# Performance work log

Measured on AMD Instinct MI355X. Metric: run time of the kernel, lower is better.

## Reference

```python
import jax, jax.numpy as jnp
import numpy as np

B, L, D = 32, 1024, 768          # batch, max wordpiece len, hidden size
C, K = 256, 8                    # max_chunk_number, max_chunk_len
PAD = 1                          # conv1d padding (kernel 3)


def setup_inputs() -> dict:
    key = jax.random.key(0)
    k1, k2, k3, k4 = jax.random.split(key, 4)
    token_level_features = jax.random.normal(k1, (B, L, D), jnp.float32)
    # values in [0,5): max total length per batch = 256*4 = 1024 = L (always in-bounds)
    chunk_lens = jax.random.randint(k2, (B, C), 0, 5)
    conv_w = jax.random.normal(k3, (D, D, 3), jnp.float32) * 0.02  # (out, in, kernel)
    conv_b = jax.random.normal(k4, (D,), jnp.float32) * 0.02
    return {"token_level_features": token_level_features, "chunk_lens": chunk_lens,
            "conv_w": conv_w, "conv_b": conv_b}


def reference(token_level_features, chunk_lens, conv_w, conv_b):
    Bb, Ll, Dd = token_level_features.shape
    Cc = chunk_lens.shape[1]
    # exclusive cumsum: start wordpiece offset of each chunk (advances by FULL len,
    # even when the chunk is truncated to K, matching the torch loop)
    starts = jnp.cumsum(chunk_lens, axis=1) - chunk_lens          # [B, C]
    trunc = jnp.minimum(chunk_lens, K)                            # [B, C]
    k = jnp.arange(K)
    idx = starts[:, :, None] + k[None, None, :]                   # [B, C, K]
    mask = k[None, None, :] < trunc[:, :, None]                   # [B, C, K]

    # ragged gather -> padded chunk buffer [B, C, K, D]
    bidx = jnp.arange(Bb)[:, None, None]
    gathered = jnp.where(mask[..., None],
                         token_level_features[bidx, jnp.clip(idx, 0, Ll - 1)],
                         0.0)

    # conv1d(k=3, pad=1) + relu over the chunk-length axis (dropout = identity in eval)
    x = gathered.reshape(Bb * Cc, K, Dd).transpose(0, 2, 1)       # [N, D, K]
    y = jax.lax.conv_general_dilated(x, conv_w, (1,), [(PAD, PAD)],
                                     dimension_numbers=('NCH', 'OIH', 'NCH'))
    y = jax.nn.relu(y + conv_b[None, :, None])
    y = y.transpose(0, 2, 1).reshape(Bb, Cc, K, Dd)               # [B, C, K, D]

    # scatter back to wordpiece positions; masked slots go to dump row L (discarded)
    safe_scatter = jnp.where(mask, idx, Ll)
    out = jnp.zeros((Bb, Ll + 1, Dd), token_level_features.dtype)
    out = out.at[bidx, safe_scatter].set(jnp.where(mask[..., None], y, 0.0))
    return out[:, :Ll]
```

## Files before the change

kernel.cpp:

```cpp
#include <hip/hip_runtime.h>
#include <stdint.h>

constexpr int NB   = 32;
constexpr int LLEN = 1024;
constexpr int DDIM = 768;
constexpr int CCH  = 256;
constexpr int KMAX = 8;
constexpr int KTOT = 3 * DDIM;

constexpr int BM = 128;
constexpr int BN = 128;
constexpr int BK = 64;
constexpr int NKS = KTOT / BK;
constexpr int NTILE = DDIM / BN;
constexpr int NRB = NB * LLEN / BM;

constexpr int CVT_SLICES = 32;
constexpr int ROWS_PER_SLICE = LLEN / CVT_SLICES;

constexpr size_t FLAGS_OFF = 0;
constexpr size_t FLAGS_SZ  = (size_t)NB * LLEN * sizeof(int);
constexpr size_t WP_OFF    = FLAGS_OFF + FLAGS_SZ;
constexpr size_t WP_SZ     = (size_t)NTILE * NKS * BN * BK * 2;
constexpr size_t ZP_OFF    = WP_OFF + WP_SZ;
constexpr size_t ZP_SZ     = 256;
constexpr size_t FB_OFF    = ZP_OFF + ZP_SZ;
constexpr size_t FB_SZ     = (size_t)NB * LLEN * DDIM * 2;
constexpr size_t WS_NEED   = FB_OFF + FB_SZ;

typedef __attribute__((ext_vector_type(4))) float f32x4;
typedef __bf16 bf16x8 __attribute__((ext_vector_type(8)));

__device__ inline unsigned short f2bf(float f) {
    unsigned u = __float_as_uint(f);
    u = u + 0x7FFFu + ((u >> 16) & 1u);
    return (unsigned short)(u >> 16);
}

__device__ inline void gload_lds16(const void* g, void* l) {
    __builtin_amdgcn_global_load_lds(
        (const __attribute__((address_space(1))) unsigned int*)g,
        (__attribute__((address_space(3))) unsigned int*)l, 16, 0, 0);
}

__global__ void meta_kernel(const int* __restrict__ chunk_lens, int* __restrict__ flags) {
    int b = blockIdx.x, tid = threadIdx.x;
    __shared__ int s[CCH];
    int len = chunk_lens[b * CCH + tid];
    s[tid] = len;
    __syncthreads();
    for (int off = 1; off < CCH; off <<= 1) {
        int v = (tid >= off) ? s[tid - off] : 0;
        __syncthreads();
        s[tid] += v;
        __syncthreads();
    }
    int start = s[tid] - len;
    for (int i = tid; i < LLEN; i += CCH) flags[b * LLEN + i] = 0;
    __syncthreads();
    int t = min(len, KMAX);
    for (int k = 0; k < t; ++k) {
        int p = start + k;
        if (p < LLEN)
            flags[b * LLEN + p] = 1 | (k > 0 ? 2 : 0) | (k + 1 < t ? 4 : 0);
    }
}

__global__ void meta_cvt_kernel(const int* __restrict__ chunk_lens,
                                const float* __restrict__ feat,
                                int* __restrict__ flags,
                                unsigned short* __restrict__ featbf) {
    int blk = blockIdx.x;
    int b   = blk / CVT_SLICES;
    int sl  = blk % CVT_SLICES;
    int tid = threadIdx.x;

    __shared__ int s[CCH];
    __shared__ int fl[LLEN];

    int len = chunk_lens[b * CCH + tid];
    s[tid] = len;
    for (int i = tid; i < LLEN; i += 256) fl[i] = 0;
    __syncthreads();
    for (int off = 1; off < CCH; off <<= 1) {
        int v = (tid >= off) ? s[tid - off] : 0;
        __syncthreads();
        s[tid] += v;
        __syncthreads();
    }
    int start = s[tid] - len;
    int t = min(len, KMAX);
    for (int k = 0; k < t; ++k) {
        int p = start + k;
        if (p < LLEN)
            fl[p] = 1 | (k > 0 ? 2 : 0) | (k + 1 < t ? 4 : 0);
    }
    __syncthreads();

    if (sl == 0) {
        for (int i = tid; i < LLEN; i += 256)
            flags[b * LLEN + i] = fl[i];
    }

    constexpr int CH = DDIM / 8;
    int r0 = sl * ROWS_PER_SLICE;
    for (int i = tid; i < ROWS_PER_SLICE * CH; i += 256) {
        int row = r0 + i / CH;
        if (!(fl[row] & 1)) continue;
        int c = i % CH;
        size_t base = ((size_t)(b * LLEN + row)) * DDIM + c * 8;
        f32x4 a  = *reinterpret_cast<const f32x4*>(feat + base);
        f32x4 cc = *reinterpret_cast<const f32x4*>(feat + base + 4);
        uint4 pack;
        pack.x = (unsigned)f2bf(a.x)  | ((unsigned)f2bf(a.y)  << 16);
        pack.y = (unsigned)f2bf(a.z)  | ((unsigned)f2bf(a.w)  << 16);
        pack.z = (unsigned)f2bf(cc.x) | ((unsigned)f2bf(cc.y) << 16);
        pack.w = (unsigned)f2bf(cc.z) | ((unsigned)f2bf(cc.w) << 16);
        *reinterpret_cast<uint4*>(featbf + base) = pack;
    }
}

__global__ void packw2_kernel(const float* __restrict__ conv_w, unsigned short* __restrict__ Wp,
                              unsigned int* __restrict__ zeropage) {
    if (blockIdx.x == gridDim.x - 1) {
        if (threadIdx.x < (int)(ZP_SZ / 4)) zeropage[threadIdx.x] = 0u;
        return;
    }
    int idx = blockIdx.x * 256 + threadIdx.x;
    if (idx >= NTILE * NKS * BN * 8) return;
    int m    = idx & 7;
    int nl   = (idx >> 3) & (BN - 1);
    int rest = idx >> 10;
    int ks   = rest % NKS;
    int nt   = rest / NKS;
    int n    = nt * BN + nl;
    int k0   = ks * BK + m * 8;
    int tap  = k0 / DDIM;
    int i0   = k0 % DDIM;
    const float* src = conv_w + ((size_t)n * DDIM + i0) * 3 + tap;
    unsigned wrds[4];
    #pragma unroll
    for (int j = 0; j < 4; ++j) {
        unsigned lo = f2bf(src[(2 * j) * 3]);
        unsigned hi = f2bf(src[(2 * j + 1) * 3]);
        wrds[j] = lo | (hi << 16);
    }
    size_t dst = ((size_t)(nt * NKS + ks)) * (BN * BK) + nl * BK + 8 * (m ^ (nl & 7));
    *reinterpret_cast<uint4*>(Wp + dst) = make_uint4(wrds[0], wrds[1], wrds[2], wrds[3]);
}

__global__ __launch_bounds__(256, 4) void conv_mfma3_kernel(
    const unsigned short* __restrict__ featbf, const int* __restrict__ flags,
    const unsigned short* __restrict__ Wp, const float* __restrict__ bias,
    const unsigned short* __restrict__ zeropage, float* __restrict__ out)
{
    int s    = blockIdx.x;
    int xcd  = s & 7;
    int slot = s >> 3;
    int b    = slot / NTILE;
    int nt   = slot % NTILE;
    int pblk = (xcd - b) & 7;
    int p0   = pblk * BM;
    int tid  = threadIdx.x;

    __shared__ int s_rf[BM];
    __shared__ int s_any;
    __shared__ float s_bias[BN];
    __shared__ __align__(16) unsigned char As[BM * BK * 2];
    __shared__ __align__(16) unsigned char Bs[BK * BN * 2];

    if (tid == 0) s_any = 0;
    __syncthreads();
    if (tid < BM) {
        int rf = flags[b * LLEN + p0 + tid];
        s_rf[tid] = rf;
        if (rf) atomicOr(&s_any, 1);
    }
    if (tid < BN) s_bias[tid] = bias[nt * BN + tid];
    __syncthreads();

    float* outbase = out + ((size_t)(b * LLEN + p0)) * DDIM + nt * BN;

    if (!s_any) {
        f32x4 z = {0.f, 0.f, 0.f, 0.f};
        #pragma unroll
        for (int q = 0; q < 16; ++q) {
            int flat = q * 256 + tid;
            int row = flat >> 5, c4 = flat & 31;
            *reinterpret_cast<f32x4*>(outbase + (size_t)row * DDIM + c4 * 4) = z;
        }
        return;
    }

    int w  = tid >> 6;
    int l  = tid & 63;
    int wr = w >> 1, wc = w & 1;
    int lr = l & 15, lg = l >> 4;

    int  useq[4];
    const unsigned short* rowptr[4];
    unsigned ldsoff[4];
    #pragma unroll
    for (int q = 0; q < 4; ++q) {
        int flat = q * 256 + tid;
        int row = flat >> 3, c8 = flat & 7;
        int c8s = c8 ^ (row & 7);
        int rf = s_rf[row];
        useq[q] = ((rf >> 1) & 1) | ((rf & 1) << 1) | (((rf >> 2) & 1) << 2);
        rowptr[q] = featbf + ((size_t)(b * LLEN + p0 + row) * DDIM + c8s * 8);
        ldsoff[q] = (unsigned)(((q * 256) + (tid & 192)) * 16);
    }
    const unsigned short* WpBase = Wp + (size_t)nt * NKS * (BN * BK) + (size_t)tid * 8;

    auto stage = [&](int ks) {
        int tap = ks / (DDIM / BK);
        int i0  = (ks % (DDIM / BK)) * BK;
        #pragma unroll
        for (int q = 0; q < 4; ++q) {
            const unsigned short* src = ((useq[q] >> tap) & 1)
                ? rowptr[q] + (size_t)(tap - 1) * DDIM + i0
                : zeropage;
            gload_lds16(src, &As[ldsoff[q]]);
        }
        const unsigned short* bsrc = WpBase + (size_t)ks * (BN * BK);
        #pragma unroll
        for (int q = 0; q < 4; ++q)
            gload_lds16(bsrc + q * 256 * 8, &Bs[ldsoff[q]]);
    };

    f32x4 acc[4][4];
    #pragma unroll
    for (int i = 0; i < 4; ++i)
        #pragma unroll
        for (int j = 0; j < 4; ++j) acc[i][j] = (f32x4){0.f, 0.f, 0.f, 0.f};

    unsigned abase[4], aswz[4], bbase[4], bswz[4];
    #pragma unroll
    for (int fm = 0; fm < 4; ++fm) {
        int row = wr * 64 + fm * 16 + lr;
        abase[fm] = (unsigned)(row * (BK * 2) + lg * 16);
        aswz[fm]  = ((unsigned)(row & 7) << 4);
    }
    #pragma unroll
    for (int fn = 0; fn < 4; ++fn) {
        int col = wc * 64 + fn * 16 + lr;
        bbase[fn] = (unsigned)(col * (BK * 2) + lg * 16);
        bswz[fn]  = ((unsigned)(col & 7) << 4);
    }

    auto compute = [&]() {
        #pragma unroll
        for (int kc = 0; kc < 2; ++kc) {
            bf16x8 av[4], bv[4];
            #pragma unroll
            for (int fm = 0; fm < 4; ++fm)
                av[fm] = *reinterpret_cast<const bf16x8*>(As + ((abase[fm] + kc * 64) ^ aswz[fm]));
            #pragma unroll
            for (int fn = 0; fn < 4; ++fn)
                bv[fn] = *reinterpret_cast<const bf16x8*>(Bs + ((bbase[fn] + kc * 64) ^ bswz[fn]));
            #pragma unroll
            for (int fm = 0; fm < 4; ++fm)
                #pragma unroll
                for (int fn = 0; fn < 4; ++fn)
                    acc[fm][fn] = __builtin_amdgcn_mfma_f32_16x16x32_bf16(
                        av[fm], bv[fn], acc[fm][fn], 0, 0, 0);
        }
    };

    #pragma unroll 1
    for (int ks = 0; ks < NKS; ++ks) {
        stage(ks);
        __syncthreads();
        compute();
        __syncthreads();
    }

    #pragma unroll
    for (int fm = 0; fm < 4; ++fm) {
        #pragma unroll
        for (int fn = 0; fn < 4; ++fn) {
            int colL = wc * 64 + fn * 16 + lr;
            float bn = s_bias[colL];
            #pragma unroll
            for (int j = 0; j < 4; ++j) {
                int rowL = wr * 64 + fm * 16 + lg * 4 + j;
                int rf = s_rf[rowL];
                float v = (rf & 1) ? fmaxf(acc[fm][fn][j] + bn, 0.f) : 0.f;
                outbase[(size_t)rowL * DDIM + colL] = v;
            }
        }
    }
}

__global__ __launch_bounds__(256) void conv_mfma_kernel(
    const float* __restrict__ feat, const int* __restrict__ flags,
    const unsigned short* __restrict__ Wp, const float* __restrict__ bias,
    float* __restrict__ out)
{
    int nt = blockIdx.x % NTILE;
    int rb = blockIdx.x / NTILE;
    int b  = rb / (LLEN / BM);
    int p0 = (rb % (LLEN / BM)) * BM;
    int tid = threadIdx.x;

    __shared__ int s_rf[BM];
    __shared__ int s_any;
    __shared__ float s_bias[BN];
    __shared__ __align__(16) unsigned char As[BM * BK * 2];
    __shared__ __align__(16) unsigned char Bs[BK * BN * 2];

    if (tid == 0) s_any = 0;
    __syncthreads();
    if (tid < BM) {
        int rf = flags[b * LLEN + p0 + tid];
        s_rf[tid] = rf;
        if (rf) atomicOr(&s_any, 1);
    }
    if (tid < BN) s_bias[tid] = bias[nt * BN + tid];
    __syncthreads();

    float* outbase = out + ((size_t)(b * LLEN + p0)) * DDIM + nt * BN;

    if (!s_any) {
        f32x4 z = {0.f, 0.f, 0.f, 0.f};
        #pragma unroll
        for (int q = 0; q < 16; ++q) {
            int flat = q * 256 + tid;
            int row = flat >> 5, c4 = flat & 31;
            *reinterpret_cast<f32x4*>(outbase + (size_t)row * DDIM + c4 * 4) = z;
        }
        return;
    }

    int w  = tid >> 6;
    int l  = tid & 63;
    int wr = w >> 1, wc = w & 1;
    int lr = l & 15, lg = l >> 4;

    f32x4 acc[4][4];
    #pragma unroll
    for (int i = 0; i < 4; ++i)
        #pragma unroll
        for (int j = 0; j < 4; ++j) acc[i][j] = (f32x4){0.f, 0.f, 0.f, 0.f};

    unsigned abase[4], aswz[4], bbase[4], bswz[4];
    #pragma unroll
    for (int fm = 0; fm < 4; ++fm) {
        int row = wr * 64 + fm * 16 + lr;
        abase[fm] = (unsigned)(row * (BK * 2) + lg * 16);
        aswz[fm]  = ((unsigned)(row & 7) << 4);
    }
    #pragma unroll
    for (int fn = 0; fn < 4; ++fn) {
        int col = wc * 64 + fn * 16 + lr;
        bbase[fn] = (unsigned)(col * (BK * 2) + lg * 16);
        bswz[fn]  = ((unsigned)(col & 7) << 4);
    }

    const unsigned short* WpBase = Wp + (size_t)nt * NKS * (BN * BK);

    for (int ks = 0; ks < NKS; ++ks) {
        int tap = ks / (DDIM / BK);
        int i0  = (ks % (DDIM / BK)) * BK;

        #pragma unroll
        for (int q = 0; q < 8; ++q) {
            int flat = q * 256 + tid;
            int row = flat >> 4, c4 = flat & 15;
            int rf = s_rf[row];
            int use = (tap == 0) ? ((rf >> 1) & 1) : (tap == 1) ? (rf & 1) : ((rf >> 2) & 1);
            unsigned lo = 0, hi = 0;
            if (use) {
                int p = p0 + row + tap - 1;
                const float* src = feat + ((size_t)(b * LLEN + p)) * DDIM + i0 + c4 * 4;
                f32x4 v = *reinterpret_cast<const f32x4*>(src);
                lo = (unsigned)f2bf(v.x) | ((unsigned)f2bf(v.y) << 16);
                hi = (unsigned)f2bf(v.z) | ((unsigned)f2bf(v.w) << 16);
            }
            unsigned byte = (unsigned)(row * (BK * 2) + c4 * 8);
            byte ^= ((unsigned)(row & 7) << 4);
            *reinterpret_cast<uint2*>(As + byte) = make_uint2(lo, hi);
        }

        {
            const uint4* src = reinterpret_cast<const uint4*>(WpBase + (size_t)ks * (BN * BK));
            uint4* dst = reinterpret_cast<uint4*>(Bs);
            #pragma unroll
            for (int q = 0; q < 4; ++q) {
                int f16 = q * 256 + tid;
                dst[f16] = src[f16];
            }
        }
        __syncthreads();

        #pragma unroll
        for (int kc = 0; kc < 2; ++kc) {
            bf16x8 av[4], bv[4];
            #pragma unroll
            for (int fm = 0; fm < 4; ++fm)
                av[fm] = *reinterpret_cast<const bf16x8*>(As + ((abase[fm] + kc * 64) ^ aswz[fm]));
            #pragma unroll
            for (int fn = 0; fn < 4; ++fn)
                bv[fn] = *reinterpret_cast<const bf16x8*>(Bs + ((bbase[fn] + kc * 64) ^ bswz[fn]));
            #pragma unroll
            for (int fm = 0; fm < 4; ++fm)
                #pragma unroll
                for (int fn = 0; fn < 4; ++fn)
                    acc[fm][fn] = __builtin_amdgcn_mfma_f32_16x16x32_bf16(
                        av[fm], bv[fn], acc[fm][fn], 0, 0, 0);
        }
        __syncthreads();
    }

    #pragma unroll
    for (int fm = 0; fm < 4; ++fm) {
        #pragma unroll
        for (int fn = 0; fn < 4; ++fn) {
            int colL = wc * 64 + fn * 16 + lr;
            float bn = s_bias[colL];
            #pragma unroll
            for (int j = 0; j < 4; ++j) {
                int rowL = wr * 64 + fm * 16 + lg * 4 + j;
                int rf = s_rf[rowL];
                float v = (rf & 1) ? fmaxf(acc[fm][fn][j] + bn, 0.f) : 0.f;
                outbase[(size_t)rowL * DDIM + colL] = v;
            }
        }
    }
}

extern "C" void kernel_launch(void* const* d_in, const int* in_sizes, int n_in,
                              void* d_out, int out_size, void* d_ws, size_t ws_size,
                              hipStream_t stream) {
    const float* feat = (const float*)d_in[0];
    const int*   lens = (const int*)d_in[1];
    const float* cw   = (const float*)d_in[2];
    const float* cb   = (const float*)d_in[3];
    float* outp = (float*)d_out;

    char* ws = (char*)d_ws;
    int* flags = (int*)(ws + FLAGS_OFF);
    unsigned short* Wp = (unsigned short*)(ws + WP_OFF);
    unsigned int* zeropage = (unsigned int*)(ws + ZP_OFF);

    packw2_kernel<<<(NTILE * NKS * BN * 8 + 255) / 256 + 1, 256, 0, stream>>>(cw, Wp, zeropage);

    if (ws_size >= WS_NEED) {
        unsigned short* featbf = (unsigned short*)(ws + FB_OFF);
        meta_cvt_kernel<<<NB * CVT_SLICES, 256, 0, stream>>>(lens, feat, flags, featbf);
        conv_mfma3_kernel<<<NRB * NTILE, 256, 0, stream>>>(featbf, flags, Wp, cb,
                                                           (const unsigned short*)zeropage, outp);
    } else {
        meta_kernel<<<NB, CCH, 0, stream>>>(lens, flags);
        conv_mfma_kernel<<<NRB * NTILE, 256, 0, stream>>>(feat, flags, Wp, cb, outp);
    }
}
```

Measured before the change: 97.22 us.

## Use 256x256 tiles with double-buffered LDS and interleaved prefetch in conv GEMM

Replaces the 128x128 single-buffered conv GEMM kernel with a 512-thread, 256x256-tile kernel. LDS is double-buffered and next-stage loads are issued in quarter-steps between MFMA groups, gated by vmcnt waits and barriers, with raised wave priority during the MFMA blocks. Weights are repacked for the wider N tile, and the block-to-XCD mapping is reworked. The larger tile cuts operand reloads and exposed load latency, but it lowers occupancy, raises register pressure, and yields a smaller grid (384 blocks), which may leave some compute units idle.

```diff
diff --git a/kernel.cpp b/kernel.cpp
--- a/kernel.cpp
+++ b/kernel.cpp
@@ -15,13 +15,19 @@
 constexpr int NTILE = DDIM / BN;
 constexpr int NRB = NB * LLEN / BM;
 
+constexpr int BM2 = 256;
+constexpr int BN2 = 256;
+constexpr int NKT = KTOT / BK;
+constexpr int NT2 = DDIM / BN2;
+constexpr int NRB2 = NB * (LLEN / BM2) * NT2;
+
 constexpr int CVT_SLICES = 32;
 constexpr int ROWS_PER_SLICE = LLEN / CVT_SLICES;
 
 constexpr size_t FLAGS_OFF = 0;
 constexpr size_t FLAGS_SZ  = (size_t)NB * LLEN * sizeof(int);
 constexpr size_t WP_OFF    = FLAGS_OFF + FLAGS_SZ;
-constexpr size_t WP_SZ     = (size_t)NTILE * NKS * BN * BK * 2;
+constexpr size_t WP_SZ     = (size_t)NT2 * NKT * BN2 * BK * 2;
 constexpr size_t ZP_OFF    = WP_OFF + WP_SZ;
 constexpr size_t ZP_SZ     = 256;
 constexpr size_t FB_OFF    = ZP_OFF + ZP_SZ;
@@ -120,12 +126,7 @@
     }
 }
 
-__global__ void packw2_kernel(const float* __restrict__ conv_w, unsigned short* __restrict__ Wp,
-                              unsigned int* __restrict__ zeropage) {
-    if (blockIdx.x == gridDim.x - 1) {
-        if (threadIdx.x < (int)(ZP_SZ / 4)) zeropage[threadIdx.x] = 0u;
-        return;
-    }
+__global__ void packw2_kernel(const float* __restrict__ conv_w, unsigned short* __restrict__ Wp) {
     int idx = blockIdx.x * 256 + threadIdx.x;
     if (idx >= NTILE * NKS * BN * 8) return;
     int m    = idx & 7;
@@ -149,44 +150,74 @@
     *reinterpret_cast<uint4*>(Wp + dst) = make_uint4(wrds[0], wrds[1], wrds[2], wrds[3]);
 }
 
-__global__ __launch_bounds__(256, 4) void conv_mfma3_kernel(
+__global__ void packw3_kernel(const float* __restrict__ conv_w, unsigned short* __restrict__ Wp2,
+                              unsigned int* __restrict__ zeropage) {
+    if (blockIdx.x == gridDim.x - 1) {
+        if (threadIdx.x < (int)(ZP_SZ / 4)) zeropage[threadIdx.x] = 0u;
+        return;
+    }
+    int idx = blockIdx.x * 256 + threadIdx.x;
+    if (idx >= NT2 * NKT * BN2 * 8) return;
+    int m    = idx & 7;
+    int nl   = (idx >> 3) & (BN2 - 1);
+    int rest = idx >> 11;
+    int ks   = rest % NKT;
+    int nt   = rest / NKT;
+    int n    = nt * BN2 + nl;
+    int k0   = ks * BK + m * 8;
+    int tap  = k0 / DDIM;
+    int i0   = k0 % DDIM;
+    const float* src = conv_w + ((size_t)n * DDIM + i0) * 3 + tap;
+    unsigned wrds[4];
+    #pragma unroll
+    for (int j = 0; j < 4; ++j) {
+        unsigned lo = f2bf(src[(2 * j) * 3]);
+        unsigned hi = f2bf(src[(2 * j + 1) * 3]);
+        wrds[j] = lo | (hi << 16);
+    }
+    size_t dst = ((size_t)(nt * NKT + ks)) * (BN2 * BK) + nl * BK + 8 * (m ^ (nl & 7));
+    *reinterpret_cast<uint4*>(Wp2 + dst) = make_uint4(wrds[0], wrds[1], wrds[2], wrds[3]);
+}
+
+__global__ __launch_bounds__(512, 2) void conv_mfma8_kernel(
     const unsigned short* __restrict__ featbf, const int* __restrict__ flags,
-    const unsigned short* __restrict__ Wp, const float* __restrict__ bias,
+    const unsigned short* __restrict__ Wp2, const float* __restrict__ bias,
     const unsigned short* __restrict__ zeropage, float* __restrict__ out)
 {
     int s    = blockIdx.x;
     int xcd  = s & 7;
     int slot = s >> 3;
-    int b    = slot / NTILE;
-    int nt   = slot % NTILE;
-    int pblk = (xcd - b) & 7;
-    int p0   = pblk * BM;
+    int nt   = slot % NT2;
+    int g    = slot / NT2;
+    int b    = g * 2 + (xcd >> 2);
+    int pblk = ((xcd & 3) + b) & 3;
+    int p0   = pblk * BM2;
     int tid  = threadIdx.x;
 
-    __shared__ int s_rf[BM];
+    __shared__ int s_rf[BM2];
     __shared__ int s_any;
-    __shared__ float s_bias[BN];
-    __shared__ __align__(16) unsigned char As[BM * BK * 2];
-    __shared__ __align__(16) unsigned char Bs[BK * BN * 2];
+    __shared__ float s_bias[BN2];
+    __shared__ __align__(16) unsigned char As[2][BM2 * BK * 2];
+    __shared__ __align__(16) unsigned char Bs[2][BN2 * BK * 2];
 
     if (tid == 0) s_any = 0;
     __syncthreads();
-    if (tid < BM) {
+    if (tid < BM2) {
         int rf = flags[b * LLEN + p0 + tid];
         s_rf[tid] = rf;
         if (rf) atomicOr(&s_any, 1);
     }
-    if (tid < BN) s_bias[tid] = bias[nt * BN + tid];
-    __syncthreads();
-
-    float* outbase = out + ((size_t)(b * LLEN + p0)) * DDIM + nt * BN;
+    if (tid < BN2) s_bias[tid] = bias[nt * BN2 + tid];
+    __syncthreads();
+
+    float* outbase = out + ((size_t)(b * LLEN + p0)) * DDIM + nt * BN2;
 
     if (!s_any) {
         f32x4 z = {0.f, 0.f, 0.f, 0.f};
         #pragma unroll
-        for (int q = 0; q < 16; ++q) {
-            int flat = q * 256 + tid;
-            int row = flat >> 5, c4 = flat & 31;
+        for (int q = 0; q < 32; ++q) {
+            int flat = q * 512 + tid;
+            int row = flat >> 6, c4 = flat & 63;
             *reinterpret_cast<f32x4*>(outbase + (size_t)row * DDIM + c4 * 4) = z;
         }
         return;
@@ -194,96 +225,137 @@
 
     int w  = tid >> 6;
     int l  = tid & 63;
-    int wr = w >> 1, wc = w & 1;
+    int wr = w >> 2, wc = w & 3;
     int lr = l & 15, lg = l >> 4;
 
-    int  useq[4];
-    const unsigned short* rowptr[4];
-    unsigned ldsoff[4];
-    #pragma unroll
-    for (int q = 0; q < 4; ++q) {
-        int flat = q * 256 + tid;
-        int row = flat >> 3, c8 = flat & 7;
-        int c8s = c8 ^ (row & 7);
-        int rf = s_rf[row];
-        useq[q] = ((rf >> 1) & 1) | ((rf & 1) << 1) | (((rf >> 2) & 1) << 2);
-        rowptr[q] = featbf + ((size_t)(b * LLEN + p0 + row) * DDIM + c8s * 8);
-        ldsoff[q] = (unsigned)(((q * 256) + (tid & 192)) * 16);
-    }
-    const unsigned short* WpBase = Wp + (size_t)nt * NKS * (BN * BK) + (size_t)tid * 8;
-
-    auto stage = [&](int ks) {
-        int tap = ks / (DDIM / BK);
-        int i0  = (ks % (DDIM / BK)) * BK;
-        #pragma unroll
-        for (int q = 0; q < 4; ++q) {
-            const unsigned short* src = ((useq[q] >> tap) & 1)
-                ? rowptr[q] + (size_t)(tap - 1) * DDIM + i0
+    int r_lo = tid >> 3, c8 = tid & 7;
+    int useqA[4];
+    const unsigned short* rowA[4];
+    #pragma unroll
+    for (int h2 = 0; h2 < 2; ++h2)
+        #pragma unroll
+        for (int s2 = 0; s2 < 2; ++s2) {
+            int r = h2 * 128 + s2 * 64 + r_lo;
+            int rf = s_rf[r];
+            int idx = h2 * 2 + s2;
+            useqA[idx] = ((rf >> 1) & 1) | ((rf & 1) << 1) | (((rf >> 2) & 1) << 2);
+            int c8s = c8 ^ (r & 7);
+            rowA[idx] = featbf + ((size_t)(b * LLEN + p0 + r) * DDIM + c8s * 8);
+        }
+    const unsigned short* WpB = Wp2 + (size_t)nt * NKT * (BN2 * BK);
+
+    auto stageA = [&](int t, int h2) {
+        int tap = t / 12, i0 = (t % 12) * BK;
+        unsigned char* base = As[t & 1] + h2 * (128 * BK * 2);
+        #pragma unroll
+        for (int s2 = 0; s2 < 2; ++s2) {
+            int idx = h2 * 2 + s2;
+            const unsigned short* src = ((useqA[idx] >> tap) & 1)
+                ? rowA[idx] + (size_t)(tap - 1) * DDIM + i0
                 : zeropage;
-            gload_lds16(src, &As[ldsoff[q]]);
-        }
-        const unsigned short* bsrc = WpBase + (size_t)ks * (BN * BK);
-        #pragma unroll
-        for (int q = 0; q < 4; ++q)
-            gload_lds16(bsrc + q * 256 * 8, &Bs[ldsoff[q]]);
+            gload_lds16(src, base + (s2 * 512 + tid) * 16);
+        }
     };
-
-    f32x4 acc[4][4];
-    #pragma unroll
-    for (int i = 0; i < 4; ++i)
+    auto stageB = [&](int t, int h2) {
+        const unsigned short* src = WpB + (size_t)t * (BN2 * BK) + (h2 * 1024 + tid) * 8;
+        unsigned char* base = Bs[t & 1] + h2 * (128 * BK * 2);
+        gload_lds16(src, base + tid * 16);
+        gload_lds16(src + 512 * 8, base + (512 + tid) * 16);
+    };
+    auto stage_half = [&](int T, int hidx) {
+        if (T >= NKT) return;
+        if (hidx == 0) stageB(T, 0);
+        else if (hidx == 1) stageB(T, 1);
+        else if (hidx == 2) stageA(T, 0);
+        else stageA(T, 1);
+    };
+
+    f32x4 acc[8][4];
+    #pragma unroll
+    for (int i = 0; i < 8; ++i)
         #pragma unroll
         for (int j = 0; j < 4; ++j) acc[i][j] = (f32x4){0.f, 0.f, 0.f, 0.f};
 
-    unsigned abase[4], aswz[4], bbase[4], bswz[4];
-    #pragma unroll
-    for (int fm = 0; fm < 4; ++fm) {
-        int row = wr * 64 + fm * 16 + lr;
-        abase[fm] = (unsigned)(row * (BK * 2) + lg * 16);
-        aswz[fm]  = ((unsigned)(row & 7) << 4);
+    unsigned aoff[8][2], boff[4][2];
+    #pragma unroll
+    for (int fm = 0; fm < 8; ++fm) {
+        int row = wr * 128 + fm * 16 + lr;
+        unsigned base = (unsigned)(row * (BK * 2) + lg * 16);
+        unsigned swz  = ((unsigned)(row & 7) << 4);
+        aoff[fm][0] = base ^ swz;
+        aoff[fm][1] = (base + 64) ^ swz;
     }
     #pragma unroll
     for (int fn = 0; fn < 4; ++fn) {
         int col = wc * 64 + fn * 16 + lr;
-        bbase[fn] = (unsigned)(col * (BK * 2) + lg * 16);
-        bswz[fn]  = ((unsigned)(col & 7) << 4);
-    }
-
-    auto compute = [&]() {
-        #pragma unroll
-        for (int kc = 0; kc < 2; ++kc) {
-            bf16x8 av[4], bv[4];
-            #pragma unroll
-            for (int fm = 0; fm < 4; ++fm)
-                av[fm] = *reinterpret_cast<const bf16x8*>(As + ((abase[fm] + kc * 64) ^ aswz[fm]));
-            #pragma unroll
-            for (int fn = 0; fn < 4; ++fn)
-                bv[fn] = *reinterpret_cast<const bf16x8*>(Bs + ((bbase[fn] + kc * 64) ^ bswz[fn]));
-            #pragma unroll
-            for (int fm = 0; fm < 4; ++fm)
+        unsigned base = (unsigned)(col * (BK * 2) + lg * 16);
+        unsigned swz  = ((unsigned)(col & 7) << 4);
+        boff[fn][0] = base ^ swz;
+        boff[fn][1] = (base + 64) ^ swz;
+    }
+
+    bf16x8 bv[4][2];
+
+    stage_half(0, 0); stage_half(0, 1); stage_half(0, 2); stage_half(0, 3);
+    stage_half(1, 0); stage_half(1, 1);
+    asm volatile("s_waitcnt vmcnt(4)" ::: "memory");
+    __builtin_amdgcn_s_barrier();
+
+    #pragma unroll 1
+    for (int t = 0; t < NKT; ++t) {
+        const unsigned char* Ab = As[t & 1];
+        const unsigned char* Bb = Bs[t & 1];
+        #pragma unroll
+        for (int q = 0; q < 4; ++q) {
+            bf16x8 av[2][2];
+            if (q == 0) {
                 #pragma unroll
                 for (int fn = 0; fn < 4; ++fn)
-                    acc[fm][fn] = __builtin_amdgcn_mfma_f32_16x16x32_bf16(
-                        av[fm], bv[fn], acc[fm][fn], 0, 0, 0);
-        }
-    };
-
-    #pragma unroll 1
-    for (int ks = 0; ks < NKS; ++ks) {
-        stage(ks);
-        __syncthreads();
-        compute();
-        __syncthreads();
-    }
-
-    #pragma unroll
-    for (int fm = 0; fm < 4; ++fm) {
+                    #pragma unroll
+                    for (int kc = 0; kc < 2; ++kc)
+                        bv[fn][kc] = *reinterpret_cast<const bf16x8*>(Bb + boff[fn][kc]);
+            }
+            #pragma unroll
+            for (int f2 = 0; f2 < 2; ++f2)
+                #pragma unroll
+                for (int kc = 0; kc < 2; ++kc)
+                    av[f2][kc] = *reinterpret_cast<const bf16x8*>(Ab + aoff[2 * q + f2][kc]);
+
+            if (q == 0)      stage_half(t + 1, 2);
+            else if (q == 1) stage_half(t + 1, 3);
+            else if (q == 2) stage_half(t + 2, 0);
+            else             stage_half(t + 2, 1);
+
+            __builtin_amdgcn_s_barrier();
+            asm volatile("s_waitcnt lgkmcnt(0)" ::: "memory");
+            __builtin_amdgcn_sched_barrier(0);
+            __builtin_amdgcn_s_setprio(1);
+            #pragma unroll
+            for (int f2 = 0; f2 < 2; ++f2)
+                #pragma unroll
+                for (int fn = 0; fn < 4; ++fn)
+                    #pragma unroll
+                    for (int kc = 0; kc < 2; ++kc)
+                        acc[2 * q + f2][fn] = __builtin_amdgcn_mfma_f32_16x16x32_bf16(
+                            av[f2][kc], bv[fn][kc], acc[2 * q + f2][fn], 0, 0, 0);
+            __builtin_amdgcn_s_setprio(0);
+            if (q == 3) {
+                if (t + 2 < NKT) asm volatile("s_waitcnt vmcnt(4)" ::: "memory");
+                else             asm volatile("s_waitcnt vmcnt(0)" ::: "memory");
+            }
+            __builtin_amdgcn_s_barrier();
+        }
+    }
+
+    #pragma unroll
+    for (int fm = 0; fm < 8; ++fm) {
         #pragma unroll
         for (int fn = 0; fn < 4; ++fn) {
             int colL = wc * 64 + fn * 16 + lr;
             float bn = s_bias[colL];
             #pragma unroll
             for (int j = 0; j < 4; ++j) {
-                int rowL = wr * 64 + fm * 16 + lg * 4 + j;
+                int rowL = wr * 128 + fm * 16 + lg * 4 + j;
                 int rf = s_rf[rowL];
                 float v = (rf & 1) ? fmaxf(acc[fm][fn][j] + bn, 0.f) : 0.f;
                 outbase[(size_t)rowL * DDIM + colL] = v;
@@ -443,15 +515,15 @@
     unsigned short* Wp = (unsigned short*)(ws + WP_OFF);
     unsigned int* zeropage = (unsigned int*)(ws + ZP_OFF);
 
-    packw2_kernel<<<(NTILE * NKS * BN * 8 + 255) / 256 + 1, 256, 0, stream>>>(cw, Wp, zeropage);
-
     if (ws_size >= WS_NEED) {
         unsigned short* featbf = (unsigned short*)(ws + FB_OFF);
+        packw3_kernel<<<(NT2 * NKT * BN2 * 8 + 255) / 256 + 1, 256, 0, stream>>>(cw, Wp, zeropage);
         meta_cvt_kernel<<<NB * CVT_SLICES, 256, 0, stream>>>(lens, feat, flags, featbf);
-        conv_mfma3_kernel<<<NRB * NTILE, 256, 0, stream>>>(featbf, flags, Wp, cb,
-                                                           (const unsigned short*)zeropage, outp);
+        conv_mfma8_kernel<<<NRB2, 512, 0, stream>>>(featbf, flags, Wp, cb,
+                                                    (const unsigned short*)zeropage, outp);
     } else {
         meta_kernel<<<NB, CCH, 0, stream>>>(lens, flags);
+        packw2_kernel<<<(NTILE * NKS * BN * 8 + 255) / 256, 256, 0, stream>>>(cw, Wp);
         conv_mfma_kernel<<<NRB * NTILE, 256, 0, stream>>>(feat, flags, Wp, cb, outp);
     }
 }
```

Measured after the change: 160.4 us. +65.0%, slower.
